# Kernel tuning notes

Measured on AMD Instinct MI355X. Metric: run time of the kernel, lower is better.

Reference implementation:

```python
import jax, jax.numpy as jnp
import numpy as np

B, S, D, H = 2, 2048, 1024, 16
DK = D // H
LN_EPS = 1e-5


def setup_inputs() -> dict:
    key = jax.random.key(0)
    ks = jax.random.split(key, 10)
    scale = 1.0 / np.sqrt(D)
    return {
        "input_Q": jax.random.normal(ks[0], (B, S, D), jnp.float32),
        "input_K": jax.random.normal(ks[1], (B, S, D), jnp.float32),
        "input_V": jax.random.normal(ks[2], (B, S, D), jnp.float32),
        "mask": jax.random.randint(ks[3], (B, S, S), 0, 2, jnp.int32),
        "W_Q": jax.random.normal(ks[4], (D, D), jnp.float32) * scale,
        "W_K": jax.random.normal(ks[5], (D, D), jnp.float32) * scale,
        "W_V": jax.random.normal(ks[6], (D, D), jnp.float32) * scale,
        "W_O": jax.random.normal(ks[7], (D, D), jnp.float32) * scale,
        "ln_gamma": jnp.ones((D,), jnp.float32),
        "ln_beta": jnp.zeros((D,), jnp.float32),
    }


def reference(input_Q, input_K, input_V, mask, W_Q, W_K, W_V, W_O, ln_gamma, ln_beta):
    # projections -> [B, H, S, DK]
    q = (input_Q @ W_Q).reshape(B, S, H, DK).transpose(0, 2, 1, 3)
    k = (input_K @ W_K).reshape(B, S, H, DK).transpose(0, 2, 1, 3)
    v = (input_V @ W_V).reshape(B, S, H, DK).transpose(0, 2, 1, 3)

    # explicit O(S^2) scores as in the original module
    scores = jnp.einsum("bhqd,bhkd->bhqk", q, k) / np.sqrt(DK)
    scores = jnp.where(mask[:, None, :, :].astype(bool), -1e9, scores)
    attn = jax.nn.softmax(scores, axis=-1)
    ctx = jnp.einsum("bhqk,bhkd->bhqd", attn, v)

    # merge heads, output projection, residual + LayerNorm
    ctx = ctx.transpose(0, 2, 1, 3).reshape(B, S, D)
    out = ctx @ W_O + input_Q
    mu = out.mean(-1, keepdims=True)
    var = jnp.mean((out - mu) ** 2, -1, keepdims=True)
    return (out - mu) * jax.lax.rsqrt(var + LN_EPS) * ln_gamma + ln_beta
```

## Files before the change

kernel.cpp:

```cpp
#include <hip/hip_runtime.h>

typedef __bf16 bf16x8 __attribute__((ext_vector_type(8)));
typedef float  f32x4  __attribute__((ext_vector_type(4)));

#define AS1 __attribute__((address_space(1)))
#define AS3 __attribute__((address_space(3)))

__device__ __forceinline__ void g2l16(const void* g, void* l) {
  __builtin_amdgcn_global_load_lds((AS1 void*)g, (AS3 void*)l, 16, 0, 0);
}
#define MFMA16(a, b, c) __builtin_amdgcn_mfma_f32_16x16x32_bf16(a, b, c, 0, 0, 0)

__device__ __forceinline__ unsigned pack_bf16(float a, float b) {
  union { __bf16 h[2]; unsigned u; } p;
  p.h[0] = (__bf16)a; p.h[1] = (__bf16)b;
  return p.u;
}

__global__ __launch_bounds__(256) void prep(const float* __restrict__ inQ,
    const float* __restrict__ inK, const float* __restrict__ inV,
    const int* __restrict__ mask,
    const float* __restrict__ W0, const float* __restrict__ W1,
    const float* __restrict__ W2, const float* __restrict__ W3,
    __bf16* __restrict__ Xq, __bf16* __restrict__ Xk, __bf16* __restrict__ Xv,
    unsigned long long* __restrict__ bits, __bf16* __restrict__ Wt) {
  __shared__ __bf16 tile[64][65];
  const int blk = blockIdx.x;
  if (blk < 6144) {
    const int z = blk >> 11, bx = blk & 2047;
    const float* src = z == 0 ? inQ : (z == 1 ? inK : inV);
    __bf16* dst = z == 0 ? Xq : (z == 1 ? Xk : Xv);
    size_t base = ((size_t)bx * 256 + threadIdx.x) * 8;
    float4 f0 = *(const float4*)(src + base);
    float4 f1 = *(const float4*)(src + base + 4);
    bf16x8 o;
    o[0] = (__bf16)f0.x; o[1] = (__bf16)f0.y; o[2] = (__bf16)f0.z; o[3] = (__bf16)f0.w;
    o[4] = (__bf16)f1.x; o[5] = (__bf16)f1.y; o[6] = (__bf16)f1.z; o[7] = (__bf16)f1.w;
    *(bf16x8*)(dst + base) = o;
  } else if (blk < 10240) {
    const int lane = threadIdx.x & 63, w = threadIdx.x >> 6;
    const int base = (blk - 6144) * 2048 + w * 512;
#pragma unroll
    for (int it = 0; it < 8; ++it) {
      int i = base + it * 64 + lane;
      unsigned long long bb = __ballot(mask[i] != 0);
      if (lane == 0) bits[i >> 6] = bb;
    }
  } else {
    const int idx = blk - 10240;
    const int z = idx >> 8, rem = idx & 255, bx = rem & 15, by = rem >> 4;
    const float* srcs[4] = {W0, W1, W2, W3};
    const float* src = srcs[z];
    __bf16* dst = Wt + (size_t)z * 1024 * 1024;
    int cb = bx * 64, rb = by * 64;
    for (int i = threadIdx.x; i < 4096; i += 256) {
      int r = i >> 6, c = i & 63;
      tile[r][c] = (__bf16)src[(size_t)(rb + r) * 1024 + cb + c];
    }
    __syncthreads();
    for (int i = threadIdx.x; i < 4096; i += 256) {
      int c = i >> 6, r = i & 63;
      dst[(size_t)(cb + c) * 1024 + rb + r] = tile[r][c];
    }
  }
}

__global__ __launch_bounds__(256) void qkv_gemm(const __bf16* __restrict__ Xq,
    const __bf16* __restrict__ Xk, const __bf16* __restrict__ Xv,
    const __bf16* __restrict__ Wt, __bf16* __restrict__ Qb,
    __bf16* __restrict__ Kb, __bf16* __restrict__ Vtb) {
  __shared__ __align__(16) __bf16 sh[8192];
  __bf16* As = sh;
  __bf16* Bs = sh + 4096;
  const int z = blockIdx.z;
  const __bf16* X = z == 0 ? Xq : (z == 1 ? Xk : Xv);
  const __bf16* W = Wt + (size_t)z * 1048576;
  const float scale = z == 0 ? 0.125f * 1.44269504088896f : 1.f;
  const int t = threadIdx.x;
  const int lane = t & 63, w = t >> 6;
  const int lane15 = lane & 15, quad = lane >> 4;
  const int wm = (w >> 1) * 64, wn = (w & 1) * 64;
  const int mBase = blockIdx.y * 128, nBase = blockIdx.x * 128;
  const int c1 = t, c2 = t + 256;
  f32x4 acc[4][4] = {};
  for (int kt = 0; kt < 1024; kt += 32) {
    __syncthreads();
    g2l16(X + (size_t)(mBase + (c1 >> 2)) * 1024 + kt + (c1 & 3) * 8, As + c1 * 8);
    g2l16(X + (size_t)(mBase + (c2 >> 2)) * 1024 + kt + (c2 & 3) * 8, As + c2 * 8);
    g2l16(W + (size_t)(nBase + (c1 >> 2)) * 1024 + kt + (c1 & 3) * 8, Bs + c1 * 8);
    g2l16(W + (size_t)(nBase + (c2 >> 2)) * 1024 + kt + (c2 & 3) * 8, Bs + c2 * 8);
    __builtin_amdgcn_s_waitcnt(0);
    __syncthreads();
    bf16x8 a[4], b[4];
#pragma unroll
    for (int i = 0; i < 4; i++) a[i] = *(const bf16x8*)&As[(wm + i * 16 + lane15) * 32 + quad * 8];
#pragma unroll
    for (int j = 0; j < 4; j++) b[j] = *(const bf16x8*)&Bs[(wn + j * 16 + lane15) * 32 + quad * 8];
#pragma unroll
    for (int i = 0; i < 4; i++)
#pragma unroll
      for (int j = 0; j < 4; j++)
        acc[i][j] = MFMA16(a[i], b[j], acc[i][j]);
  }
  if (z != 2) {
    __bf16* Y = z == 0 ? Qb : Kb;
#pragma unroll
    for (int i = 0; i < 4; i++)
#pragma unroll
      for (int j = 0; j < 4; j++)
#pragma unroll
        for (int r = 0; r < 4; r++) {
          int mg = mBase + wm + i * 16 + quad * 4 + r;
          int ng = nBase + wn + j * 16 + lane15;
          int b_ = mg >> 11, s_ = mg & 2047, h_ = ng >> 6, d_ = ng & 63;
          Y[(((size_t)(b_ * 16 + h_)) * 2048 + s_) * 64 + d_] = (__bf16)(acc[i][j][r] * scale);
        }
  } else {
    const int s0 = mBase & 2047;
    const int bhBase = (mBase >> 11) * 16 + (nBase >> 6);
#pragma unroll
    for (int half = 0; half < 2; ++half) {
      __syncthreads();
      if ((w & 1) == half) {
#pragma unroll
        for (int i = 0; i < 4; i++)
#pragma unroll
          for (int j = 0; j < 4; j++)
#pragma unroll
            for (int r = 0; r < 4; r++) {
              int nl = j * 16 + lane15;
              int ml = wm + i * 16 + quad * 4 + r;
              sh[nl * 128 + (ml ^ ((nl & 7) * 16))] = (__bf16)acc[i][j][r];
            }
      }
      __syncthreads();
      const int row = t >> 2, c0 = (t & 3) * 32;
      const int xr = (row & 7) * 16;
      const int b0 = row * 128 + (c0 ^ xr);
      const int b1 = row * 128 + ((c0 + 16) ^ xr);
      bf16x8 a0 = *(const bf16x8*)&sh[b0];
      bf16x8 a1 = *(const bf16x8*)&sh[b0 + 8];
      bf16x8 a2 = *(const bf16x8*)&sh[b1];
      bf16x8 a3 = *(const bf16x8*)&sh[b1 + 8];
      __bf16* dst = Vtb + (size_t)(bhBase + half) * 131072 + (size_t)row * 2048 + s0 + c0;
      *(bf16x8*)(dst)      = a0;
      *(bf16x8*)(dst + 8)  = a1;
      *(bf16x8*)(dst + 16) = a2;
      *(bf16x8*)(dst + 24) = a3;
    }
  }
}

__global__ __launch_bounds__(256) void gemm_wo(const __bf16* __restrict__ X,
    const __bf16* __restrict__ Wt, const float* __restrict__ resid,
    float* __restrict__ Yf) {
  __shared__ __align__(16) __bf16 As[64 * 32];
  __shared__ __align__(16) __bf16 Bs[128 * 32];
  const int t = threadIdx.x;
  const int lane = t & 63, w = t >> 6;
  const int lane15 = lane & 15, quad = lane >> 4;
  const int wm = (w >> 1) * 32, wn = (w & 1) * 64;
  const int mBase = blockIdx.y * 64, nBase = blockIdx.x * 128;
  f32x4 acc[2][4] = {};
  for (int kt = 0; kt < 1024; kt += 32) {
    __syncthreads();
    g2l16(X  + (size_t)(mBase + (t >> 2)) * 1024 + kt + (t & 3) * 8, As + t * 8);
    g2l16(Wt + (size_t)(nBase + (t >> 2)) * 1024 + kt + (t & 3) * 8, Bs + t * 8);
    g2l16(Wt + (size_t)(nBase + ((t + 256) >> 2)) * 1024 + kt + (t & 3) * 8, Bs + (t + 256) * 8);
    __builtin_amdgcn_s_waitcnt(0);
    __syncthreads();
    bf16x8 a[2], b[4];
#pragma unroll
    for (int i = 0; i < 2; i++) a[i] = *(const bf16x8*)&As[(wm + i * 16 + lane15) * 32 + quad * 8];
#pragma unroll
    for (int j = 0; j < 4; j++) b[j] = *(const bf16x8*)&Bs[(wn + j * 16 + lane15) * 32 + quad * 8];
#pragma unroll
    for (int i = 0; i < 2; i++)
#pragma unroll
      for (int j = 0; j < 4; j++)
        acc[i][j] = MFMA16(a[i], b[j], acc[i][j]);
  }
#pragma unroll
  for (int i = 0; i < 2; i++)
#pragma unroll
    for (int j = 0; j < 4; j++)
#pragma unroll
      for (int r = 0; r < 4; r++) {
        int mg = mBase + wm + i * 16 + quad * 4 + r;
        int ng = nBase + wn + j * 16 + lane15;
        size_t idx = (size_t)mg * 1024 + ng;
        Yf[idx] = acc[i][j][r] + resid[idx];
      }
}

__global__ __launch_bounds__(256) void attn_kernel(const __bf16* __restrict__ Q,
    const __bf16* __restrict__ Kp, const __bf16* __restrict__ Vt,
    const unsigned* __restrict__ mbits, __bf16* __restrict__ ctx) {
  __shared__ __align__(16) __bf16 Qs[64 * 64];
  __shared__ __align__(16) __bf16 Ks[2][32 * 64];
  __shared__ __align__(16) __bf16 Vs[4][64 * 32];
  __shared__ __align__(16) __bf16 Ps[4][2][16 * 32];
  const int t = threadIdx.x, lane = t & 63, w = t >> 6;
  const int l15 = lane & 15, quad = lane >> 4;
  const int psw = (l15 >> 1) & 3;
  const int bh = blockIdx.y, b = bh >> 4, h = bh & 15;
  const int qBase = blockIdx.x * 64;
  const size_t qko = (size_t)bh * 2048 * 64;
  const size_t vko = (size_t)bh * 64 * 2048;
  const int srow8 = lane >> 3, sch8 = (lane & 7) ^ srow8;
  const int srow16 = lane >> 2, sch4 = (lane & 3) ^ ((lane >> 3) & 3);
  g2l16(Q + qko + (size_t)(qBase + w * 8 + srow8) * 64 + sch8 * 8,       Qs + w * 512 + lane * 8);
  g2l16(Q + qko + (size_t)(qBase + (w + 4) * 8 + srow8) * 64 + sch8 * 8, Qs + (w + 4) * 512 + lane * 8);
  g2l16(Kp + qko + (size_t)(w * 8 + srow8) * 64 + sch8 * 8,     &Ks[0][0] + w * 512 + lane * 8);
  g2l16(Vt + vko + (size_t)(w * 16 + srow16) * 2048 + sch4 * 8, &Vs[0][0] + w * 512 + lane * 8);
  const size_t mIdx = ((size_t)b * 2048 + qBase + w * 16 + l15) * 64;
  unsigned m32 = mbits[mIdx];
  __builtin_amdgcn_s_waitcnt(0);
  __syncthreads();
  bf16x8 qb0, qb1;
  {
    const int r = w * 16 + l15, s = r & 7;
    qb0 = *(const bf16x8*)&Qs[r * 64 + ((quad ^ s) * 8)];
    qb1 = *(const bf16x8*)&Qs[r * 64 + (((4 + quad) ^ s) * 8)];
  }
  bf16x8 ones;
#pragma unroll
  for (int i = 0; i < 8; i++) ones[i] = (__bf16)1.0f;
  f32x4 o[4] = {};
  f32x4 ol = {};
  bf16x8 pa_prev;
#pragma unroll 4
  for (int kt = 0; kt < 64; ++kt) {
    __syncthreads();
    unsigned mnext = 0;
    if (kt < 63) {
      const int tB = (kt + 1) * 32;
      g2l16(Kp + qko + (size_t)(tB + w * 8 + srow8) * 64 + sch8 * 8,     &Ks[(kt + 1) & 1][0] + w * 512 + lane * 8);
      g2l16(Vt + vko + (size_t)(w * 16 + srow16) * 2048 + tB + sch4 * 8, &Vs[(kt + 1) & 3][0] + w * 512 + lane * 8);
      mnext = mbits[mIdx + kt + 1];
    }
    f32x4 st[2];
#pragma unroll
    for (int j = 0; j < 2; j++) {
      const int tr = j * 16 + l15, s = tr & 7;
      bf16x8 ka0 = *(const bf16x8*)&Ks[kt & 1][tr * 64 + ((quad ^ s) * 8)];
      bf16x8 ka1 = *(const bf16x8*)&Ks[kt & 1][tr * 64 + (((4 + quad) ^ s) * 8)];
      f32x4 zz = {0.f, 0.f, 0.f, 0.f};
      zz = MFMA16(ka0, qb0, zz);
      st[j] = MFMA16(ka1, qb1, zz);
    }
    if (kt > 0) {
      const __bf16* Vb = &Vs[(kt - 1) & 3][0];
      ol = MFMA16(pa_prev, ones, ol);
#pragma unroll
      for (int j = 0; j < 4; j++) {
        const int dr = j * 16 + l15;
        bf16x8 vb = *(const bf16x8*)&Vb[dr * 32 + ((quad ^ ((dr >> 1) & 3)) * 8)];
        o[j] = MFMA16(pa_prev, vb, o[j]);
      }
    }
    __bf16* Pw = &Ps[w][kt & 1][0];
#pragma unroll
    for (int j = 0; j < 2; j++) {
      const int t0 = j * 16 + quad * 4;
      float e0 = ((m32 >> (t0 + 0)) & 1u) ? 0.f : __builtin_exp2f(st[j][0]);
      float e1 = ((m32 >> (t0 + 1)) & 1u) ? 0.f : __builtin_exp2f(st[j][1]);
      float e2 = ((m32 >> (t0 + 2)) & 1u) ? 0.f : __builtin_exp2f(st[j][2]);
      float e3 = ((m32 >> (t0 + 3)) & 1u) ? 0.f : __builtin_exp2f(st[j][3]);
      const int ch = t0 >> 3;
      char* pbase = (char*)Pw + l15 * 64 + ((ch ^ psw) * 16) + ((t0 & 7) * 2);
      *(unsigned*)(pbase)     = pack_bf16(e0, e1);
      *(unsigned*)(pbase + 4) = pack_bf16(e2, e3);
    }
    m32 = mnext;
    __builtin_amdgcn_s_waitcnt(0xC07F);
    pa_prev = *(const bf16x8*)&Pw[l15 * 32 + ((quad ^ psw) * 8)];
  }
  {
    const __bf16* Vb = &Vs[63 & 3][0];
    ol = MFMA16(pa_prev, ones, ol);
#pragma unroll
    for (int j = 0; j < 4; j++) {
      const int dr = j * 16 + l15;
      bf16x8 vb = *(const bf16x8*)&Vb[dr * 32 + ((quad ^ ((dr >> 1) & 3)) * 8)];
      o[j] = MFMA16(pa_prev, vb, o[j]);
    }
  }
#pragma unroll
  for (int r = 0; r < 4; r++) {
    float inv = 1.f / ol[r];
    int qg = qBase + w * 16 + quad * 4 + r;
    size_t base = ((size_t)b * 2048 + qg) * 1024 + h * 64;
#pragma unroll
    for (int j = 0; j < 4; j++)
      ctx[base + j * 16 + l15] = (__bf16)(o[j][r] * inv);
  }
}

__global__ __launch_bounds__(256) void ln_kernel(const float* __restrict__ X,
    const float* __restrict__ gamma, const float* __restrict__ beta,
    float* __restrict__ out) {
  __shared__ float red[8];
  const int t = threadIdx.x;
  const size_t row = blockIdx.x;
  const float* xr = X + row * 1024;
  float4 x = *(const float4*)(xr + t * 4);
  float s = x.x + x.y + x.z + x.w;
  float s2 = x.x * x.x + x.y * x.y + x.z * x.z + x.w * x.w;
#pragma unroll
  for (int off = 1; off < 64; off <<= 1) { s += __shfl_xor(s, off); s2 += __shfl_xor(s2, off); }
  if ((t & 63) == 0) { red[t >> 6] = s; red[4 + (t >> 6)] = s2; }
  __syncthreads();
  float S1 = red[0] + red[1] + red[2] + red[3];
  float S2 = red[4] + red[5] + red[6] + red[7];
  float mu = S1 * (1.f / 1024.f);
  float var = S2 * (1.f / 1024.f) - mu * mu;
  float rs = rsqrtf(var + 1e-5f);
  float4 g = *(const float4*)(gamma + t * 4);
  float4 bb = *(const float4*)(beta + t * 4);
  float4 y;
  y.x = (x.x - mu) * rs * g.x + bb.x;
  y.y = (x.y - mu) * rs * g.y + bb.y;
  y.z = (x.z - mu) * rs * g.z + bb.z;
  y.w = (x.w - mu) * rs * g.w + bb.w;
  *(float4*)(out + row * 1024 + t * 4) = y;
}

extern "C" void kernel_launch(void* const* d_in, const int* in_sizes, int n_in,
                              void* d_out, int out_size, void* d_ws, size_t ws_size,
                              hipStream_t stream) {
  const float* inQ  = (const float*)d_in[0];
  const float* inK  = (const float*)d_in[1];
  const float* inV  = (const float*)d_in[2];
  const int*   mask = (const int*)d_in[3];
  const float* WQ   = (const float*)d_in[4];
  const float* WK   = (const float*)d_in[5];
  const float* WV   = (const float*)d_in[6];
  const float* WO   = (const float*)d_in[7];
  const float* gamma = (const float*)d_in[8];
  const float* beta  = (const float*)d_in[9];

  const size_t MB = 1024 * 1024;
  char* ws = (char*)d_ws;
  __bf16* Xq  = (__bf16*)(ws);
  __bf16* Xk  = (__bf16*)(ws + 8 * MB);
  __bf16* Xv  = (__bf16*)(ws + 16 * MB);
  __bf16* Qb  = (__bf16*)(ws + 24 * MB);
  __bf16* Kb  = (__bf16*)(ws + 32 * MB);
  __bf16* Vtb = (__bf16*)(ws + 48 * MB);
  __bf16* Wt  = (__bf16*)(ws + 56 * MB);
  unsigned long long* mbits = (unsigned long long*)(ws + 64 * MB);
  __bf16* ctx  = Xq;
  float*  outp = (float*)(ws + 8 * MB);

  prep<<<dim3(11264), 256, 0, stream>>>(inQ, inK, inV, mask, WQ, WK, WV, WO,
                                        Xq, Xk, Xv, mbits, Wt);
  qkv_gemm<<<dim3(8, 32, 3), 256, 0, stream>>>(Xq, Xk, Xv, Wt, Qb, Kb, Vtb);
  attn_kernel<<<dim3(32, 32), 256, 0, stream>>>(Qb, Kb, Vtb, (const unsigned*)mbits, ctx);
  gemm_wo<<<dim3(8, 64), 256, 0, stream>>>(ctx, Wt + 3 * 1048576, inQ, outp);
  ln_kernel<<<dim3(4096), 256, 0, stream>>>(outp, gamma, beta, (float*)d_out);
}
```

Baseline: 307.9 us.

## Keep softmax probabilities in registers by permuting V key layout

The attention kernel no longer stages exponentiated scores through shared memory to reshape them into the MFMA A-operand layout. Each lane now packs its own exp values directly into the bf16x8 operand, and the V-transpose write in the projection kernel permutes key order within 32-key groups so the register layout lines up with the V tiles. The mask bits are inverted so a branchless AND can zero masked entries. This removes an LDS write/read round trip and a waitcnt per key tile, but it depends on three pieces staying consistent: the permuted V layout, the inverted mask, and the matching P register layout.

```diff
diff --git a/kernel.cpp b/kernel.cpp
--- a/kernel.cpp
+++ b/kernel.cpp
@@ -43,7 +43,7 @@
 #pragma unroll
     for (int it = 0; it < 8; ++it) {
       int i = base + it * 64 + lane;
-      unsigned long long bb = __ballot(mask[i] != 0);
+      unsigned long long bb = __ballot(mask[i] == 0);
       if (lane == 0) bits[i >> 6] = bb;
     }
   } else {
@@ -130,7 +130,9 @@
             for (int r = 0; r < 4; r++) {
               int nl = j * 16 + lane15;
               int ml = wm + i * 16 + quad * 4 + r;
-              sh[nl * 128 + (ml ^ ((nl & 7) * 16))] = (__bf16)acc[i][j][r];
+              int l5 = ml & 31;
+              int mlp = (ml & 96) | ((((l5 >> 2) & 3) * 8) + (l5 & 3) + (((l5 >> 4) & 1) * 4));
+              sh[nl * 128 + (mlp ^ ((nl & 7) * 16))] = (__bf16)acc[i][j][r];
             }
       }
       __syncthreads();
@@ -199,10 +201,8 @@
   __shared__ __align__(16) __bf16 Qs[64 * 64];
   __shared__ __align__(16) __bf16 Ks[2][32 * 64];
   __shared__ __align__(16) __bf16 Vs[4][64 * 32];
-  __shared__ __align__(16) __bf16 Ps[4][2][16 * 32];
   const int t = threadIdx.x, lane = t & 63, w = t >> 6;
   const int l15 = lane & 15, quad = lane >> 4;
-  const int psw = (l15 >> 1) & 3;
   const int bh = blockIdx.y, b = bh >> 4, h = bh & 15;
   const int qBase = blockIdx.x * 64;
   const size_t qko = (size_t)bh * 2048 * 64;
@@ -259,22 +259,24 @@
         o[j] = MFMA16(pa_prev, vb, o[j]);
       }
     }
-    __bf16* Pw = &Ps[w][kt & 1][0];
-#pragma unroll
-    for (int j = 0; j < 2; j++) {
-      const int t0 = j * 16 + quad * 4;
-      float e0 = ((m32 >> (t0 + 0)) & 1u) ? 0.f : __builtin_exp2f(st[j][0]);
-      float e1 = ((m32 >> (t0 + 1)) & 1u) ? 0.f : __builtin_exp2f(st[j][1]);
-      float e2 = ((m32 >> (t0 + 2)) & 1u) ? 0.f : __builtin_exp2f(st[j][2]);
-      float e3 = ((m32 >> (t0 + 3)) & 1u) ? 0.f : __builtin_exp2f(st[j][3]);
-      const int ch = t0 >> 3;
-      char* pbase = (char*)Pw + l15 * 64 + ((ch ^ psw) * 16) + ((t0 & 7) * 2);
-      *(unsigned*)(pbase)     = pack_bf16(e0, e1);
-      *(unsigned*)(pbase + 4) = pack_bf16(e2, e3);
+    {
+      const unsigned msh = m32 >> (quad * 4);
+      union { unsigned u[4]; bf16x8 v; } pk;
+#pragma unroll
+      for (int j = 0; j < 2; j++) {
+        float e[4];
+#pragma unroll
+        for (int r = 0; r < 4; r++) {
+          int sel = ((int)(msh << (31 - (j * 16 + r)))) >> 31;
+          float ev = __builtin_exp2f(st[j][r]);
+          e[r] = __uint_as_float(__float_as_uint(ev) & (unsigned)sel);
+        }
+        pk.u[2 * j]     = pack_bf16(e[0], e[1]);
+        pk.u[2 * j + 1] = pack_bf16(e[2], e[3]);
+      }
+      pa_prev = pk.v;
     }
     m32 = mnext;
-    __builtin_amdgcn_s_waitcnt(0xC07F);
-    pa_prev = *(const bf16x8*)&Pw[l15 * 32 + ((quad ^ psw) * 8)];
   }
   {
     const __bf16* Vb = &Vs[63 & 3][0];
```

Measured after the change: 284.9 us. 7.5% less time.
